# Performance work log

Measured on AMD Instinct MI355X. Metric: run time of the kernel, lower is better.

The kernel has to match this reference:

```python
import jax, jax.numpy as jnp
import numpy as np

NA, NP, NT = 100000, 200000, 50000      # authors, papers, terms
DA, DP, DT = 128, 128, 64               # input feature dims per node type
E_AP, E_PA, E_TP, E_PT = 400000, 400000, 300000, 300000
H, OUT = 64, 4                          # hidden_channels, out_channels
NEG_SLOPE = 0.01                        # nn.LeakyReLU default


def setup_inputs() -> dict:
    keys = iter(jax.random.split(jax.random.key(0), 64))
    rn = lambda shape, s=0.05: jax.random.normal(next(keys), shape, dtype=jnp.float32) * s
    ri = lambda n, hi: jax.random.randint(next(keys), (n,), 0, hi, dtype=jnp.int32)
    inp = {
        'x_author': rn((NA, DA), 1.0),
        'x_paper': rn((NP, DP), 1.0),
        'x_term': rn((NT, DT), 1.0),
        'src_ap': ri(E_AP, NA), 'dst_ap': ri(E_AP, NP),
        'src_pa': ri(E_PA, NP), 'dst_pa': ri(E_PA, NA),
        'src_tp': ri(E_TP, NT), 'dst_tp': ri(E_TP, NP),
        'src_pt': ri(E_PT, NP), 'dst_pt': ri(E_PT, NT),
    }
    # SAGEConv params per edge type: Wl (on mean-aggregated src feats, with bias),
    # Wr (root/dst feats, no bias) -- matches PyG SAGEConv(lin_l, lin_r).
    dims = {'ap': (DA, DP), 'pa': (DP, DA), 'tp': (DT, DP), 'pt': (DP, DT)}
    for et, (ds, dd) in dims.items():
        inp['l1_' + et + '_Wl'] = rn((ds, H))
        inp['l1_' + et + '_bl'] = rn((H,))
        inp['l1_' + et + '_Wr'] = rn((dd, H))
        inp['l2_' + et + '_Wl'] = rn((H, H))
        inp['l2_' + et + '_bl'] = rn((H,))
        inp['l2_' + et + '_Wr'] = rn((H, H))
    inp['lin_W'] = rn((H, OUT))
    inp['lin_b'] = rn((OUT,))
    return inp


def _sage(x_src, x_dst, src, dst, Wl, bl, Wr):
    """PyG SAGEConv (mean aggr): lin_l(mean_j x_src[j]) + lin_r(x_dst)."""
    n_dst = x_dst.shape[0]
    agg = jax.ops.segment_sum(x_src[src], dst, num_segments=n_dst)        # [n_dst, d_src]
    cnt = jax.ops.segment_sum(jnp.ones_like(dst, dtype=x_src.dtype), dst, num_segments=n_dst)
    mean = agg / jnp.maximum(cnt, 1.0)[:, None]
    return mean @ Wl + bl + x_dst @ Wr


def reference(x_author, x_paper, x_term,
              src_ap, dst_ap, src_pa, dst_pa, src_tp, dst_tp, src_pt, dst_pt,
              l1_ap_Wl, l1_ap_bl, l1_ap_Wr, l1_pa_Wl, l1_pa_bl, l1_pa_Wr,
              l1_tp_Wl, l1_tp_bl, l1_tp_Wr, l1_pt_Wl, l1_pt_bl, l1_pt_Wr,
              l2_ap_Wl, l2_ap_bl, l2_ap_Wr, l2_pa_Wl, l2_pa_bl, l2_pa_Wr,
              l2_tp_Wl, l2_tp_bl, l2_tp_Wr, l2_pt_Wl, l2_pt_bl, l2_pt_Wr,
              lin_W, lin_b):
    lrelu = lambda v: jax.nn.leaky_relu(v, NEG_SLOPE)
    # Layer 1 (HeteroConv, sum across relations into each dst type) + LeakyReLU.
    p1 = lrelu(_sage(x_author, x_paper, src_ap, dst_ap, l1_ap_Wl, l1_ap_bl, l1_ap_Wr)
               + _sage(x_term, x_paper, src_tp, dst_tp, l1_tp_Wl, l1_tp_bl, l1_tp_Wr))
    a1 = lrelu(_sage(x_paper, x_author, src_pa, dst_pa, l1_pa_Wl, l1_pa_bl, l1_pa_Wr))
    # (term output of layer 1 / layer-2 paper & term outputs do not reach the
    # returned 'author' logits -- omitted, exactly as autograd would prune them.)
    # Layer 2: author output only needs paper->author relation.
    a2 = _sage(p1, a1, src_pa, dst_pa, l2_pa_Wl, l2_pa_bl, l2_pa_Wr)
    return a2 @ lin_W + lin_b  # [NA, OUT]
```

## Files before the change

kernel.cpp:

```cpp
#include <hip/hip_runtime.h>

#define NA 100000
#define NP 200000
#define NT 50000
#define E_AP 400000
#define E_PA 400000
#define E_TP 300000
#define E_TOT (E_AP + E_TP + E_PA)
#define HD 64
#define NOUT 4
#define NEG 0.01f
#define M_CNT (2 * NP + NA)
#define SCAN_NB ((M_CNT + 1023) / 1024)

typedef __attribute__((ext_vector_type(8))) short bf16x8;
typedef __attribute__((ext_vector_type(4))) float f32x4;

static __device__ __forceinline__ short f2bf(float f) {
  unsigned u = __float_as_uint(f);
  unsigned r = (u + 0x7FFFu + ((u >> 16) & 1u)) >> 16;
  return (short)r;
}
static __device__ __forceinline__ float bflo(unsigned u) {
  return __uint_as_float(u << 16);
}
static __device__ __forceinline__ float bfhi(unsigned u) {
  return __uint_as_float(u & 0xFFFF0000u);
}

static __device__ __forceinline__ void acc8(float* acc, uint4 u, float w) {
  acc[0] = fmaf(w, bflo(u.x), acc[0]);
  acc[1] = fmaf(w, bfhi(u.x), acc[1]);
  acc[2] = fmaf(w, bflo(u.y), acc[2]);
  acc[3] = fmaf(w, bfhi(u.y), acc[3]);
  acc[4] = fmaf(w, bflo(u.z), acc[4]);
  acc[5] = fmaf(w, bfhi(u.z), acc[5]);
  acc[6] = fmaf(w, bflo(u.w), acc[6]);
  acc[7] = fmaf(w, bfhi(u.w), acc[7]);
}

#define R_NP 16384
#define R_NA 32768
#define R_TP 36864
#define R_BLC 36928
#define R_WFL 37184
#define R_WFR 37440
#define R_BF 37444
#define BZ_NB ((M_CNT / 4 + 255) / 256)
__global__ __launch_bounds__(256) void build_zero_kernel(
    const float* __restrict__ l1_ap_Wl, const float* __restrict__ l1_ap_bl,
    const float* __restrict__ l1_ap_Wr,
    const float* __restrict__ l1_pa_Wl, const float* __restrict__ l1_pa_bl,
    const float* __restrict__ l1_pa_Wr,
    const float* __restrict__ l1_tp_Wl, const float* __restrict__ l1_tp_bl,
    const float* __restrict__ l1_tp_Wr,
    const float* __restrict__ l2_Wl, const float* __restrict__ l2_bl,
    const float* __restrict__ l2_Wr,
    const float* __restrict__ lin_W, const float* __restrict__ lin_b,
    short* __restrict__ Wt_np, short* __restrict__ Wt_na, short* __restrict__ Wt_tp,
    float* __restrict__ blc, float* __restrict__ Wfl, float* __restrict__ Wfr,
    float* __restrict__ bf, int* __restrict__ cnt) {
  int t = blockIdx.x * 256 + threadIdx.x;
  int z4 = t * 4;
  if (z4 < M_CNT) *(int4*)(cnt + z4) = make_int4(0, 0, 0, 0);

  if (t < R_NP) {
    int c = t >> 7, k = t & 127;
    float v = (c < 64) ? l1_pa_Wl[k * 64 + c]
                       : (l1_ap_Wr[k * 64 + (c - 64)] + l1_tp_Wr[k * 64 + (c - 64)]);
    Wt_np[t] = f2bf(v);
  } else if (t < R_NA) {
    int i = t - R_NP;
    int c = i >> 7, k = i & 127;
    float v = (c < 64) ? l1_ap_Wl[k * 64 + c] : l1_pa_Wr[k * 64 + (c - 64)];
    Wt_na[i] = f2bf(v);
  } else if (t < R_TP) {
    int i = t - R_NA;
    int c = i >> 6, k = i & 63;
    Wt_tp[i] = f2bf(l1_tp_Wl[k * 64 + c]);
  } else if (t < R_BLC) {
    int c = t - R_TP;
    blc[c] = l1_ap_bl[c] + l1_tp_bl[c];
  } else if (t < R_WFL) {
    int i = t - R_BLC;
    int k = i >> 2, c = i & 3;
    float s = 0.f;
    for (int j = 0; j < HD; ++j) s += l2_Wl[k * HD + j] * lin_W[j * NOUT + c];
    Wfl[i] = s;
  } else if (t < R_WFR) {
    int i = t - R_WFL;
    int k = i >> 2, c = i & 3;
    float s = 0.f;
    for (int j = 0; j < HD; ++j) s += l2_Wr[k * HD + j] * lin_W[j * NOUT + c];
    Wfr[i] = s;
  } else if (t < R_BF) {
    int c = t - R_WFR;
    float s = lin_b[c];
    for (int j = 0; j < HD; ++j) s += l2_bl[j] * lin_W[j * NOUT + c];
    bf[c] = s;
  }
}

__global__ __launch_bounds__(256) void count_all(const int* __restrict__ dst_ap,
                                                 const int* __restrict__ dst_tp,
                                                 const int* __restrict__ dst_pa,
                                                 int* __restrict__ cnt) {
  int i4 = (blockIdx.x * 256 + threadIdx.x) * 4;
  const int* p;
  int base;
  if (i4 < E_AP) { p = dst_ap + i4; base = 0; }
  else if (i4 < E_AP + E_TP) { p = dst_tp + (i4 - E_AP); base = NP; }
  else if (i4 < E_TOT) { p = dst_pa + (i4 - E_AP - E_TP); base = 2 * NP; }
  else return;
  int4 d = *(const int4*)p;
  atomicAdd(&cnt[base + d.x], 1);
  atomicAdd(&cnt[base + d.y], 1);
  atomicAdd(&cnt[base + d.z], 1);
  atomicAdd(&cnt[base + d.w], 1);
}

__global__ __launch_bounds__(256) void scan1(const int* __restrict__ cnt,
                                             int* __restrict__ offs,
                                             int* __restrict__ bsum) {
  __shared__ int ts[256];
  int t = threadIdx.x;
  int idx = blockIdx.x * 1024 + t * 4;
  int4 v = make_int4(0, 0, 0, 0);
  if (idx < M_CNT) v = *(const int4*)(cnt + idx);
  int s = v.x + v.y + v.z + v.w;
  ts[t] = s;
  __syncthreads();
  for (int off = 1; off < 256; off <<= 1) {
    int a = (t >= off) ? ts[t - off] : 0;
    __syncthreads();
    ts[t] += a;
    __syncthreads();
  }
  int excl = ts[t] - s;
  if (idx < M_CNT) {
    int4 o;
    o.x = excl; o.y = o.x + v.x; o.z = o.y + v.y; o.w = o.z + v.z;
    *(int4*)(offs + idx) = o;
  }
  if (t == 255) bsum[blockIdx.x] = ts[255];
}

__global__ __launch_bounds__(256) void scan2(int* __restrict__ bsum, int nb) {
  __shared__ int ts[256];
  __shared__ int carrysh;
  int t = threadIdx.x;
  int carry = 0;
  for (int base = 0; base < nb; base += 256) {
    int v = (base + t < nb) ? bsum[base + t] : 0;
    ts[t] = v;
    __syncthreads();
    for (int off = 1; off < 256; off <<= 1) {
      int a = (t >= off) ? ts[t - off] : 0;
      __syncthreads();
      ts[t] += a;
      __syncthreads();
    }
    if (base + t < nb) bsum[base + t] = carry + ts[t] - v;
    if (t == 255) carrysh = ts[255];
    __syncthreads();
    carry += carrysh;
    __syncthreads();
  }
}

__global__ __launch_bounds__(256) void scan3(int* __restrict__ offs,
                                             const int* __restrict__ bsum) {
  int add = bsum[blockIdx.x];
  int idx = blockIdx.x * 1024 + threadIdx.x * 4;
  if (idx < M_CNT) {
    int4 v = *(const int4*)(offs + idx);
    v.x += add; v.y += add; v.z += add; v.w += add;
    *(int4*)(offs + idx) = v;
  }
}

__global__ __launch_bounds__(256) void bucket_kernel(
    const int* __restrict__ src_ap, const int* __restrict__ dst_ap,
    const int* __restrict__ src_tp, const int* __restrict__ dst_tp,
    const int* __restrict__ src_pa, const int* __restrict__ dst_pa,
    int* __restrict__ offs, int* __restrict__ ebuf) {
  int i4 = (blockIdx.x * 256 + threadIdx.x) * 4;
  const int *sp, *dp;
  int base;
  if (i4 < E_AP) { sp = src_ap + i4; dp = dst_ap + i4; base = 0; }
  else if (i4 < E_AP + E_TP) { int j = i4 - E_AP; sp = src_tp + j; dp = dst_tp + j; base = NP; }
  else if (i4 < E_TOT) { int j = i4 - E_AP - E_TP; sp = src_pa + j; dp = dst_pa + j; base = 2 * NP; }
  else return;
  int4 s = *(const int4*)sp;
  int4 d = *(const int4*)dp;
  ebuf[atomicAdd(&offs[base + d.x], 1)] = s.x;
  ebuf[atomicAdd(&offs[base + d.y], 1)] = s.y;
  ebuf[atomicAdd(&offs[base + d.z], 1)] = s.z;
  ebuf[atomicAdd(&offs[base + d.w], 1)] = s.w;
}

template <int K, int COLS, bool HAS_OUT1>
static __device__ __forceinline__ void gemm_body(const float* __restrict__ X,
                                                 const short* __restrict__ Wt,
                                                 const float* __restrict__ bias1,
                                                 unsigned short* __restrict__ out0,
                                                 unsigned short* __restrict__ out1,
                                                 int N, int bid,
                                                 unsigned short* __restrict__ lds) {
  constexpr int NSTEP = K / 32;
  constexpr int NTILE = COLS / 16;
  constexpr int WROWB = K * 2;
  constexpr int WBYTES = COLS * K * 2;
  const int t = threadIdx.x;
  const int lane = t & 63;
  const int w = t >> 6;
  const int m = lane & 15;
  const int quad = lane >> 4;

  const int r0 = bid * 128 + w * 16;
  const int r1 = r0 + 64;
  bf16x8 a0[NSTEP], a1[NSTEP];
  {
    const float* x0 = X + (size_t)min(r0 + m, N - 1) * K + quad * 8;
    const float* x1 = X + (size_t)min(r1 + m, N - 1) * K + quad * 8;
#pragma unroll
    for (int s = 0; s < NSTEP; ++s) {
      float4 v0 = *(const float4*)(x0 + s * 32);
      float4 v1 = *(const float4*)(x0 + s * 32 + 4);
      float4 u0 = *(const float4*)(x1 + s * 32);
      float4 u1 = *(const float4*)(x1 + s * 32 + 4);
      bf16x8 a;
      a[0] = f2bf(v0.x); a[1] = f2bf(v0.y); a[2] = f2bf(v0.z); a[3] = f2bf(v0.w);
      a[4] = f2bf(v1.x); a[5] = f2bf(v1.y); a[6] = f2bf(v1.z); a[7] = f2bf(v1.w);
      a0[s] = a;
      bf16x8 b;
      b[0] = f2bf(u0.x); b[1] = f2bf(u0.y); b[2] = f2bf(u0.z); b[3] = f2bf(u0.w);
      b[4] = f2bf(u1.x); b[5] = f2bf(u1.y); b[6] = f2bf(u1.z); b[7] = f2bf(u1.w);
      a1[s] = b;
    }
  }

  {
    const char* wsrc = (const char*)Wt;
    char* wdst = (char*)lds;
#pragma unroll
    for (int i = 0; i < WBYTES / 4096; ++i) {
      const int byte = t * 16 + i * 4096;
      const uint4 v = *(const uint4*)(wsrc + byte);
      const int row = byte / WROWB;
      *(uint4*)(wdst + (byte ^ ((row & 7) << 4))) = v;
    }
  }
  __syncthreads();

  f32x4 acc0[NTILE], acc1[NTILE];
#pragma unroll
  for (int ct = 0; ct < NTILE; ++ct) {
    acc0[ct] = (f32x4){0.f, 0.f, 0.f, 0.f};
    acc1[ct] = (f32x4){0.f, 0.f, 0.f, 0.f};
  }
#pragma unroll
  for (int ct = 0; ct < NTILE; ++ct) {
    const int wrow = ct * 16 + m;
    const int swx = (wrow & 7) << 4;
#pragma unroll
    for (int s = 0; s < NSTEP; ++s) {
      const int byte = wrow * WROWB + s * 64 + quad * 16;
      const bf16x8 b = *(const bf16x8*)((const char*)lds + (byte ^ swx));
      acc0[ct] = __builtin_amdgcn_mfma_f32_16x16x32_bf16(a0[s], b, acc0[ct], 0, 0, 0);
      acc1[ct] = __builtin_amdgcn_mfma_f32_16x16x32_bf16(a1[s], b, acc1[ct], 0, 0, 0);
    }
  }
  __syncthreads();

  constexpr int OROWB = COLS * 2;
#pragma unroll
  for (int ct = 0; ct < NTILE; ++ct) {
    const int col = ct * 16 + m;
    const float add = (HAS_OUT1 && ct >= NTILE / 2) ? bias1[col - 64] : 0.f;
#pragma unroll
    for (int rg = 0; rg < 4; ++rg) {
      const int lr0 = w * 16 + quad * 4 + rg;
      const int lr1 = lr0 + 64;
      const int b0 = lr0 * OROWB + col * 2;
      const int b1 = lr1 * OROWB + col * 2;
      *(unsigned short*)((char*)lds + (b0 ^ ((lr0 & 7) << 4))) =
          (unsigned short)f2bf(acc0[ct][rg] + add);
      *(unsigned short*)((char*)lds + (b1 ^ ((lr1 & 7) << 4))) =
          (unsigned short)f2bf(acc1[ct][rg] + add);
    }
  }
  __syncthreads();

  constexpr int OUTB = 128 * OROWB;
#pragma unroll
  for (int i = 0; i < OUTB / 4096; ++i) {
    const int byte = t * 16 + i * 4096;
    const int row = byte / OROWB;
    const int colb = byte - row * OROWB;
    const uint4 v = *(const uint4*)((const char*)lds + (byte ^ ((row & 7) << 4)));
    const int grow = bid * 128 + row;
    if (grow < N) {
      unsigned short* dst = (HAS_OUT1 && colb >= 128) ? out1 : out0;
      *(uint4*)((char*)dst + (size_t)grow * (HD * 2) + (colb & 127)) = v;
    }
  }
}

#define GB_P ((NP + 127) / 128)
#define GB_A ((NA + 127) / 128)
#define GB_T ((NT + 127) / 128)

__global__ __launch_bounds__(256, 4) void gemm_all(
    const float* __restrict__ x_paper, const float* __restrict__ x_author,
    const float* __restrict__ x_term,
    const short* __restrict__ Wt_np, const short* __restrict__ Wt_na,
    const short* __restrict__ Wt_tp,
    const float* __restrict__ blc, const float* __restrict__ l1_pa_bl,
    unsigned short* __restrict__ yp, unsigned short* __restrict__ P1root,
    unsigned short* __restrict__ ya, unsigned short* __restrict__ A1root,
    unsigned short* __restrict__ yt) {
  __shared__ unsigned short lds[16384];
  int b = blockIdx.x;
  if (b < GB_P) {
    gemm_body<128, 128, true>(x_paper, Wt_np, blc, yp, P1root, NP, b, lds);
  } else if (b < GB_P + GB_A) {
    gemm_body<128, 128, true>(x_author, Wt_na, l1_pa_bl, ya, A1root, NA, b - GB_P, lds);
  } else {
    gemm_body<64, 64, false>(x_term, Wt_tp, nullptr, yt, nullptr, NT, b - GB_P - GB_A, lds);
  }
}

__global__ __launch_bounds__(256) void paper_agg(
    const unsigned short* __restrict__ ya, const unsigned short* __restrict__ yt,
    const unsigned short* __restrict__ P1root,
    const int* __restrict__ cnt, const int* __restrict__ offs,
    const int* __restrict__ ebuf, const float* __restrict__ Wfl,
    float* __restrict__ z) {
  const int wv = threadIdx.x >> 6;
  const int lane = threadIdx.x & 63;
  const int g = lane >> 3;
  const int l = lane & 7;
  const int p = blockIdx.x * 32 + wv * 8 + g;
  const bool pv = p < NP;
  const int pc = pv ? p : NP - 1;

  const int cA = cnt[pc], cT = cnt[NP + pc];
  const int startA = offs[pc] - cA;
  const int startT = offs[NP + pc] - cT;

  const unsigned short* yab = ya + 8 * l;
  const unsigned short* ytb = yt + 8 * l;

  float accA[8], accT[8];
#pragma unroll
  for (int j = 0; j < 8; ++j) { accA[j] = 0.f; accT[j] = 0.f; }

  const int mx = max(cA, cT);
  for (int i = 0; i < mx; i += 2) {
    const bool a0 = i < cA, a1 = i + 1 < cA;
    const bool t0 = i < cT, t1 = i + 1 < cT;
    int sA0 = ebuf[startA + i];
    int sA1 = ebuf[startA + i + 1];
    int sT0 = ebuf[startT + i];
    int sT1 = ebuf[startT + i + 1];
    sA0 = a0 ? sA0 : 0;
    sA1 = a1 ? sA1 : 0;
    sT0 = t0 ? sT0 : 0;
    sT1 = t1 ? sT1 : 0;
    const uint4 uA0 = *(const uint4*)(yab + (size_t)sA0 * HD);
    const uint4 uA1 = *(const uint4*)(yab + (size_t)sA1 * HD);
    const uint4 uT0 = *(const uint4*)(ytb + (size_t)sT0 * HD);
    const uint4 uT1 = *(const uint4*)(ytb + (size_t)sT1 * HD);
    acc8(accA, uA0, a0 ? 1.f : 0.f);
    acc8(accA, uA1, a1 ? 1.f : 0.f);
    acc8(accT, uT0, t0 ? 1.f : 0.f);
    acc8(accT, uT1, t1 ? 1.f : 0.f);
  }

  const float rA = 1.0f / (float)max(cA, 1);
  const float rT = 1.0f / (float)max(cT, 1);
  uint4 rt = *(const uint4*)(P1root + (size_t)pc * HD + 8 * l);
  float v[8];
  v[0] = bflo(rt.x); v[1] = bfhi(rt.x); v[2] = bflo(rt.y); v[3] = bfhi(rt.y);
  v[4] = bflo(rt.z); v[5] = bfhi(rt.z); v[6] = bflo(rt.w); v[7] = bfhi(rt.w);
  float4 pz = make_float4(0.f, 0.f, 0.f, 0.f);
#pragma unroll
  for (int j = 0; j < 8; ++j) {
    float x = v[j] + accA[j] * rA + accT[j] * rT;
    x = fmaxf(x, NEG * x);
    float4 wf = *(const float4*)(Wfl + (8 * l + j) * 4);
    pz.x += x * wf.x; pz.y += x * wf.y; pz.z += x * wf.z; pz.w += x * wf.w;
  }
#pragma unroll
  for (int m = 1; m < 8; m <<= 1) {
    pz.x += __shfl_xor(pz.x, m);
    pz.y += __shfl_xor(pz.y, m);
    pz.z += __shfl_xor(pz.z, m);
    pz.w += __shfl_xor(pz.w, m);
  }
  if (l == 0 && pv) *(float4*)(z + (size_t)p * NOUT) = pz;
}

__global__ __launch_bounds__(256) void author_agg(
    const unsigned short* __restrict__ yp, const unsigned short* __restrict__ A1root,
    const float* __restrict__ z,
    const int* __restrict__ cnt, const int* __restrict__ offs,
    const int* __restrict__ ebuf, const float* __restrict__ Wfr,
    const float* __restrict__ bf, float* __restrict__ out) {
  const int wv = threadIdx.x >> 6;
  const int lane = threadIdx.x & 63;
  const int g = lane >> 3;
  const int l = lane & 7;
  const int a = blockIdx.x * 32 + wv * 8 + g;
  const bool av = a < NA;
  const int ac = av ? a : NA - 1;

  const int c = cnt[2 * NP + ac];
  const int start = offs[2 * NP + ac] - c;

  const unsigned short* ypb = yp + 8 * l;

  float acc[8];
#pragma unroll
  for (int j = 0; j < 8; ++j) acc[j] = 0.f;
  float4 az = make_float4(0.f, 0.f, 0.f, 0.f);

  for (int i = 0; i < c; i += 2) {
    const bool b1 = i + 1 < c;
    int s0 = ebuf[start + i];
    int s1 = ebuf[min(start + i + 1, E_TOT - 1)];
    s1 = b1 ? s1 : 0;
    const uint4 u0 = *(const uint4*)(ypb + (size_t)s0 * HD);
    const uint4 u1 = *(const uint4*)(ypb + (size_t)s1 * HD);
    const float4 z0 = *(const float4*)(z + (size_t)s0 * NOUT);
    const float4 z1 = *(const float4*)(z + (size_t)s1 * NOUT);
    const float w1 = b1 ? 1.f : 0.f;
    acc8(acc, u0, 1.f);
    acc8(acc, u1, w1);
    az.x = fmaf(w1, z1.x, az.x + z0.x);
    az.y = fmaf(w1, z1.y, az.y + z0.y);
    az.z = fmaf(w1, z1.z, az.z + z0.z);
    az.w = fmaf(w1, z1.w, az.w + z0.w);
  }

  const float r = 1.0f / (float)max(c, 1);
  uint4 rt = *(const uint4*)(A1root + (size_t)ac * HD + 8 * l);
  float v[8];
  v[0] = bflo(rt.x); v[1] = bfhi(rt.x); v[2] = bflo(rt.y); v[3] = bfhi(rt.y);
  v[4] = bflo(rt.z); v[5] = bfhi(rt.z); v[6] = bflo(rt.w); v[7] = bfhi(rt.w);
  float4 o = make_float4(0.f, 0.f, 0.f, 0.f);
#pragma unroll
  for (int j = 0; j < 8; ++j) {
    float x = v[j] + acc[j] * r;
    x = fmaxf(x, NEG * x);
    float4 wf = *(const float4*)(Wfr + (8 * l + j) * 4);
    o.x += x * wf.x; o.y += x * wf.y; o.z += x * wf.z; o.w += x * wf.w;
  }
#pragma unroll
  for (int m = 1; m < 8; m <<= 1) {
    o.x += __shfl_xor(o.x, m);
    o.y += __shfl_xor(o.y, m);
    o.z += __shfl_xor(o.z, m);
    o.w += __shfl_xor(o.w, m);
  }
  if (l == 0 && av) {
    float4 b = *(const float4*)bf;
    o.x += az.x * r + b.x;
    o.y += az.y * r + b.y;
    o.z += az.z * r + b.z;
    o.w += az.w * r + b.w;
    *(float4*)(out + (size_t)a * NOUT) = o;
  }
}

extern "C" void kernel_launch(void* const* d_in, const int* in_sizes, int n_in,
                              void* d_out, int out_size, void* d_ws, size_t ws_size,
                              hipStream_t stream) {
  const float* x_author = (const float*)d_in[0];
  const float* x_paper  = (const float*)d_in[1];
  const float* x_term   = (const float*)d_in[2];
  const int* src_ap = (const int*)d_in[3];
  const int* dst_ap = (const int*)d_in[4];
  const int* src_pa = (const int*)d_in[5];
  const int* dst_pa = (const int*)d_in[6];
  const int* src_tp = (const int*)d_in[7];
  const int* dst_tp = (const int*)d_in[8];
  const float* l1_ap_Wl = (const float*)d_in[11];
  const float* l1_ap_bl = (const float*)d_in[12];
  const float* l1_ap_Wr = (const float*)d_in[13];
  const float* l1_pa_Wl = (const float*)d_in[17];
  const float* l1_pa_bl = (const float*)d_in[18];
  const float* l1_pa_Wr = (const float*)d_in[19];
  const float* l2_pa_Wl = (const float*)d_in[20];
  const float* l2_pa_bl = (const float*)d_in[21];
  const float* l2_pa_Wr = (const float*)d_in[22];
  const float* l1_tp_Wl = (const float*)d_in[23];
  const float* l1_tp_bl = (const float*)d_in[24];
  const float* l1_tp_Wr = (const float*)d_in[25];
  const float* lin_W = (const float*)d_in[35];
  const float* lin_b = (const float*)d_in[36];
  float* out = (float*)d_out;

  char* wsb = (char*)d_ws;
  auto carve = [&](size_t bytes) {
    char* p = wsb;
    wsb += (bytes + 15) & ~(size_t)15;
    return p;
  };
  unsigned short* ya = (unsigned short*)carve((size_t)NA * HD * 2);
  unsigned short* yp = (unsigned short*)carve((size_t)NP * HD * 2);
  unsigned short* yt = (unsigned short*)carve((size_t)NT * HD * 2);
  unsigned short* P1root = (unsigned short*)carve((size_t)NP * HD * 2);
  unsigned short* A1root = (unsigned short*)carve((size_t)NA * HD * 2);
  float* z = (float*)carve((size_t)NP * NOUT * 4);
  int* cnt = (int*)carve((size_t)M_CNT * 4);
  int* offs = (int*)carve((size_t)M_CNT * 4);
  int* bsum = (int*)carve((size_t)SCAN_NB * 4);
  int* ebuf = (int*)carve((size_t)E_TOT * 4);
  short* Wt_np = (short*)carve(128 * 128 * 2);
  short* Wt_na = (short*)carve(128 * 128 * 2);
  short* Wt_tp = (short*)carve(64 * 64 * 2);
  float* blc = (float*)carve(HD * 4);
  float* Wfl = (float*)carve(HD * NOUT * 4);
  float* Wfr = (float*)carve(HD * NOUT * 4);
  float* bf  = (float*)carve(NOUT * 4);

  build_zero_kernel<<<BZ_NB, 256, 0, stream>>>(
      l1_ap_Wl, l1_ap_bl, l1_ap_Wr, l1_pa_Wl, l1_pa_bl, l1_pa_Wr,
      l1_tp_Wl, l1_tp_bl, l1_tp_Wr, l2_pa_Wl, l2_pa_bl, l2_pa_Wr,
      lin_W, lin_b, Wt_np, Wt_na, Wt_tp, blc, Wfl, Wfr, bf, cnt);
  count_all<<<(E_TOT / 4 + 255) / 256, 256, 0, stream>>>(dst_ap, dst_tp, dst_pa, cnt);

  scan1<<<SCAN_NB, 256, 0, stream>>>(cnt, offs, bsum);
  scan2<<<1, 256, 0, stream>>>(bsum, SCAN_NB);
  scan3<<<SCAN_NB, 256, 0, stream>>>(offs, bsum);

  gemm_all<<<GB_P + GB_A + GB_T, 256, 0, stream>>>(
      x_paper, x_author, x_term, Wt_np, Wt_na, Wt_tp, blc, l1_pa_bl,
      yp, P1root, ya, A1root, yt);

  bucket_kernel<<<(E_TOT / 4 + 255) / 256, 256, 0, stream>>>(src_ap, dst_ap, src_tp, dst_tp,
                                                             src_pa, dst_pa, offs, ebuf);

  paper_agg<<<(NP + 31) / 32, 256, 0, stream>>>(ya, yt, P1root, cnt, offs, ebuf, Wfl, z);
  author_agg<<<(NA + 31) / 32, 256, 0, stream>>>(yp, A1root, z, cnt, offs, ebuf, Wfr, bf, out);
}
```

Before: 469.8 us.

## Make node-feature GEMM persistent with double-buffered row-tile prefetch

Replaces the one-block-per-128-row GEMM with a persistent kernel of 768 blocks, split across paper, author and term in fixed ratios. Each block loads the weight matrix into LDS once and loops over 64-row tiles. It prefetches the next tile's fp32 rows into registers while computing the current one, and each warp stages its output through a private LDS region without block-wide barriers. The goal is to amortise the weight staging and hide global-load latency, at the cost of more registers (launch bounds drop to 3 blocks per SM), more LDS, and possible imbalance from the fixed block split.

```diff
diff --git a/kernel.cpp b/kernel.cpp
--- a/kernel.cpp
+++ b/kernel.cpp
@@ -200,45 +200,93 @@
 }
 
 template <int K, int COLS, bool HAS_OUT1>
-static __device__ __forceinline__ void gemm_body(const float* __restrict__ X,
-                                                 const short* __restrict__ Wt,
-                                                 const float* __restrict__ bias1,
-                                                 unsigned short* __restrict__ out0,
-                                                 unsigned short* __restrict__ out1,
-                                                 int N, int bid,
-                                                 unsigned short* __restrict__ lds) {
+static __device__ __forceinline__ void gemm_persist(
+    const float* __restrict__ X, const short* __restrict__ Wt,
+    const float* __restrict__ bias1,
+    unsigned short* __restrict__ out0, unsigned short* __restrict__ out1,
+    int N, int nt, int bidp, int nb, unsigned short* __restrict__ lds) {
   constexpr int NSTEP = K / 32;
   constexpr int NTILE = COLS / 16;
   constexpr int WROWB = K * 2;
   constexpr int WBYTES = COLS * K * 2;
+  constexpr int OROWB = COLS * 2;
+  constexpr int OWB = 16 * COLS * 2;
   const int t = threadIdx.x;
   const int lane = t & 63;
   const int w = t >> 6;
   const int m = lane & 15;
   const int quad = lane >> 4;
 
-  const int r0 = bid * 128 + w * 16;
-  const int r1 = r0 + 64;
-  bf16x8 a0[NSTEP], a1[NSTEP];
-  {
-    const float* x0 = X + (size_t)min(r0 + m, N - 1) * K + quad * 8;
-    const float* x1 = X + (size_t)min(r1 + m, N - 1) * K + quad * 8;
+  unsigned short* outw = lds + WBYTES / 2 + w * (OWB / 2);
+
+  float4 rawA[2 * NSTEP], rawB[2 * NSTEP];
+  float badd[HAS_OUT1 ? NTILE / 2 : 1];
+
+  auto LOADRAW = [&](float4* buf, int tile) {
+    const int row = tile * 64 + w * 16 + m;
+    const float* xr = X + (size_t)min(row, N - 1) * K + quad * 8;
 #pragma unroll
     for (int s = 0; s < NSTEP; ++s) {
-      float4 v0 = *(const float4*)(x0 + s * 32);
-      float4 v1 = *(const float4*)(x0 + s * 32 + 4);
-      float4 u0 = *(const float4*)(x1 + s * 32);
-      float4 u1 = *(const float4*)(x1 + s * 32 + 4);
+      buf[2 * s] = *(const float4*)(xr + s * 32);
+      buf[2 * s + 1] = *(const float4*)(xr + s * 32 + 4);
+    }
+  };
+
+  auto COMPUTE = [&](float4* buf, int tile) {
+    bf16x8 af[NSTEP];
+#pragma unroll
+    for (int s = 0; s < NSTEP; ++s) {
+      float4 v0 = buf[2 * s], v1 = buf[2 * s + 1];
       bf16x8 a;
       a[0] = f2bf(v0.x); a[1] = f2bf(v0.y); a[2] = f2bf(v0.z); a[3] = f2bf(v0.w);
       a[4] = f2bf(v1.x); a[5] = f2bf(v1.y); a[6] = f2bf(v1.z); a[7] = f2bf(v1.w);
-      a0[s] = a;
-      bf16x8 b;
-      b[0] = f2bf(u0.x); b[1] = f2bf(u0.y); b[2] = f2bf(u0.z); b[3] = f2bf(u0.w);
-      b[4] = f2bf(u1.x); b[5] = f2bf(u1.y); b[6] = f2bf(u1.z); b[7] = f2bf(u1.w);
-      a1[s] = b;
-    }
-  }
+      af[s] = a;
+    }
+    f32x4 acc[NTILE];
+#pragma unroll
+    for (int ct = 0; ct < NTILE; ++ct) acc[ct] = (f32x4){0.f, 0.f, 0.f, 0.f};
+#pragma unroll
+    for (int ct = 0; ct < NTILE; ++ct) {
+      const int wrow = ct * 16 + m;
+      const int swx = (wrow & 7) << 4;
+#pragma unroll
+      for (int s = 0; s < NSTEP; ++s) {
+        const int byte = wrow * WROWB + s * 64 + quad * 16;
+        const bf16x8 b = *(const bf16x8*)((const char*)lds + (byte ^ swx));
+        acc[ct] = __builtin_amdgcn_mfma_f32_16x16x32_bf16(af[s], b, acc[ct], 0, 0, 0);
+      }
+    }
+#pragma unroll
+    for (int ct = 0; ct < NTILE; ++ct) {
+      const int col = ct * 16 + m;
+      float add = 0.f;
+      if constexpr (HAS_OUT1) {
+        if (ct >= NTILE / 2) add = badd[ct - NTILE / 2];
+      }
+#pragma unroll
+      for (int rg = 0; rg < 4; ++rg) {
+        const int r = quad * 4 + rg;
+        const int bo = r * OROWB + col * 2;
+        *(unsigned short*)((char*)outw + (bo ^ ((r & 7) << 4))) =
+            (unsigned short)f2bf(acc[ct][rg] + add);
+      }
+    }
+#pragma unroll
+    for (int i2 = 0; i2 < OWB / 1024; ++i2) {
+      const int byte = lane * 16 + i2 * 1024;
+      const int r = byte / OROWB;
+      const int colb = byte - r * OROWB;
+      const uint4 v = *(const uint4*)((const char*)outw + (byte ^ ((r & 7) << 4)));
+      const int grow = tile * 64 + w * 16 + r;
+      if (grow < N) {
+        unsigned short* dst = (HAS_OUT1 && colb >= 128) ? out1 : out0;
+        const int off = HAS_OUT1 ? (colb & 127) : colb;
+        *(uint4*)((char*)dst + (size_t)grow * (HD * 2) + off) = v;
+      }
+    }
+  };
+
+  LOADRAW(rawA, bidp);
 
   {
     const char* wsrc = (const char*)Wt;
@@ -253,65 +301,41 @@
   }
   __syncthreads();
 
-  f32x4 acc0[NTILE], acc1[NTILE];
-#pragma unroll
-  for (int ct = 0; ct < NTILE; ++ct) {
-    acc0[ct] = (f32x4){0.f, 0.f, 0.f, 0.f};
-    acc1[ct] = (f32x4){0.f, 0.f, 0.f, 0.f};
-  }
-#pragma unroll
-  for (int ct = 0; ct < NTILE; ++ct) {
-    const int wrow = ct * 16 + m;
-    const int swx = (wrow & 7) << 4;
-#pragma unroll
-    for (int s = 0; s < NSTEP; ++s) {
-      const int byte = wrow * WROWB + s * 64 + quad * 16;
-      const bf16x8 b = *(const bf16x8*)((const char*)lds + (byte ^ swx));
-      acc0[ct] = __builtin_amdgcn_mfma_f32_16x16x32_bf16(a0[s], b, acc0[ct], 0, 0, 0);
-      acc1[ct] = __builtin_amdgcn_mfma_f32_16x16x32_bf16(a1[s], b, acc1[ct], 0, 0, 0);
-    }
-  }
-  __syncthreads();
-
-  constexpr int OROWB = COLS * 2;
-#pragma unroll
-  for (int ct = 0; ct < NTILE; ++ct) {
-    const int col = ct * 16 + m;
-    const float add = (HAS_OUT1 && ct >= NTILE / 2) ? bias1[col - 64] : 0.f;
-#pragma unroll
-    for (int rg = 0; rg < 4; ++rg) {
-      const int lr0 = w * 16 + quad * 4 + rg;
-      const int lr1 = lr0 + 64;
-      const int b0 = lr0 * OROWB + col * 2;
-      const int b1 = lr1 * OROWB + col * 2;
-      *(unsigned short*)((char*)lds + (b0 ^ ((lr0 & 7) << 4))) =
-          (unsigned short)f2bf(acc0[ct][rg] + add);
-      *(unsigned short*)((char*)lds + (b1 ^ ((lr1 & 7) << 4))) =
-          (unsigned short)f2bf(acc1[ct][rg] + add);
-    }
-  }
-  __syncthreads();
-
-  constexpr int OUTB = 128 * OROWB;
-#pragma unroll
-  for (int i = 0; i < OUTB / 4096; ++i) {
-    const int byte = t * 16 + i * 4096;
-    const int row = byte / OROWB;
-    const int colb = byte - row * OROWB;
-    const uint4 v = *(const uint4*)((const char*)lds + (byte ^ ((row & 7) << 4)));
-    const int grow = bid * 128 + row;
-    if (grow < N) {
-      unsigned short* dst = (HAS_OUT1 && colb >= 128) ? out1 : out0;
-      *(uint4*)((char*)dst + (size_t)grow * (HD * 2) + (colb & 127)) = v;
-    }
-  }
-}
-
-#define GB_P ((NP + 127) / 128)
-#define GB_A ((NA + 127) / 128)
-#define GB_T ((NT + 127) / 128)
-
-__global__ __launch_bounds__(256, 4) void gemm_all(
+  if constexpr (HAS_OUT1) {
+#pragma unroll
+    for (int j = 0; j < NTILE / 2; ++j) badd[j] = bias1[j * 16 + m];
+  }
+
+  const int nit = (nt - 1 - bidp) / nb + 1;
+  int tile = bidp;
+  int i = 0;
+  for (;;) {
+    int tnext = tile + nb;
+    bool more = (i + 1 < nit);
+    if (more) LOADRAW(rawB, tnext);
+    COMPUTE(rawA, tile);
+    ++i;
+    if (!more) break;
+    tile = tnext;
+    tnext = tile + nb;
+    more = (i + 1 < nit);
+    if (more) LOADRAW(rawA, tnext);
+    COMPUTE(rawB, tile);
+    ++i;
+    if (!more) break;
+    tile = tnext;
+  }
+}
+
+#define PERS_NBLK 768
+#define PB_P 439
+#define PB_A 219
+#define PB_T (PERS_NBLK - PB_P - PB_A)
+#define PT_P ((NP + 63) / 64)
+#define PT_A ((NA + 63) / 64)
+#define PT_T ((NT + 63) / 64)
+
+__global__ __launch_bounds__(256, 3) void gemm_all(
     const float* __restrict__ x_paper, const float* __restrict__ x_author,
     const float* __restrict__ x_term,
     const short* __restrict__ Wt_np, const short* __restrict__ Wt_na,
@@ -320,14 +344,16 @@
     unsigned short* __restrict__ yp, unsigned short* __restrict__ P1root,
     unsigned short* __restrict__ ya, unsigned short* __restrict__ A1root,
     unsigned short* __restrict__ yt) {
-  __shared__ unsigned short lds[16384];
+  __shared__ unsigned short lds[24576];
   int b = blockIdx.x;
-  if (b < GB_P) {
-    gemm_body<128, 128, true>(x_paper, Wt_np, blc, yp, P1root, NP, b, lds);
-  } else if (b < GB_P + GB_A) {
-    gemm_body<128, 128, true>(x_author, Wt_na, l1_pa_bl, ya, A1root, NA, b - GB_P, lds);
+  if (b < PB_P) {
+    gemm_persist<128, 128, true>(x_paper, Wt_np, blc, yp, P1root, NP, PT_P, b, PB_P, lds);
+  } else if (b < PB_P + PB_A) {
+    gemm_persist<128, 128, true>(x_author, Wt_na, l1_pa_bl, ya, A1root, NA, PT_A,
+                                 b - PB_P, PB_A, lds);
   } else {
-    gemm_body<64, 64, false>(x_term, Wt_tp, nullptr, yt, nullptr, NT, b - GB_P - GB_A, lds);
+    gemm_persist<64, 64, false>(x_term, Wt_tp, nullptr, yt, nullptr, NT, PT_T,
+                                b - PB_P - PB_A, PB_T, lds);
   }
 }
 
@@ -536,7 +562,7 @@
   scan2<<<1, 256, 0, stream>>>(bsum, SCAN_NB);
   scan3<<<SCAN_NB, 256, 0, stream>>>(offs, bsum);
 
-  gemm_all<<<GB_P + GB_A + GB_T, 256, 0, stream>>>(
+  gemm_all<<<PERS_NBLK, 256, 0, stream>>>(
       x_paper, x_author, x_term, Wt_np, Wt_na, Wt_tp, blc, l1_pa_bl,
       yp, P1root, ya, A1root, yt);
 
```

Measured after the change: 519.9 us. 1.11x slower.
